# Kernel optimization log

Measured on AMD Instinct MI355X. Metric: run time of the kernel, lower is better.

## Reference

```python
import jax, jax.numpy as jnp
import numpy as np

N = 100000
E = 1600000
IN_CH = 128
HEADS = 4
OUT_CH = 32
NEG_SLOPE = 0.2


def setup_inputs() -> dict:
    key = jax.random.key(0)
    k1, k2, k3, k4 = jax.random.split(key, 4)
    x = jax.random.normal(k1, (N, IN_CH), dtype=jnp.float32)
    edge_index = jax.random.randint(k2, (2, E), 0, N, dtype=jnp.int64)
    # xavier-uniform-like init scales
    w_lim = float(np.sqrt(6.0 / (IN_CH + HEADS * OUT_CH)))
    a_lim = float(np.sqrt(6.0 / (HEADS + 2 * OUT_CH)))
    weight = jax.random.uniform(k3, (IN_CH, HEADS * OUT_CH), dtype=jnp.float32, minval=-w_lim, maxval=w_lim)
    att = jax.random.uniform(k4, (1, HEADS, 2 * OUT_CH), dtype=jnp.float32, minval=-a_lim, maxval=a_lim)
    bias = jnp.zeros((HEADS * OUT_CH,), dtype=jnp.float32)
    return {"x": x, "edge_index": edge_index, "weight": weight, "att": att, "bias": bias}


def reference(x, edge_index, weight, att, bias):
    n = x.shape[0]
    h = jnp.matmul(x, weight).reshape(n, HEADS, OUT_CH)  # [N, H, C]
    src, dst = edge_index[0], edge_index[1]
    x_src = h[src]  # [E, H, C]
    x_dst = h[dst]  # [E, H, C]
    # att is [1, H, 2C]; split so we never materialize the concat tensor
    att_src = att[:, :, :OUT_CH]  # [1, H, C]
    att_dst = att[:, :, OUT_CH:]  # [1, H, C]
    alpha = (x_src * att_src).sum(-1) + (x_dst * att_dst).sum(-1)  # [E, H]
    alpha = jnp.where(alpha >= 0, alpha, NEG_SLOPE * alpha)  # leaky_relu
    # segment softmax over edges grouped by dst
    seg_max = jax.ops.segment_max(alpha, dst, num_segments=n)  # [N, H]
    alpha = jnp.exp(alpha - seg_max[dst])
    seg_sum = jax.ops.segment_sum(alpha, dst, num_segments=n)  # [N, H]
    alpha = alpha / (seg_sum[dst] + 1e-16)
    # scatter-add weighted messages
    out = jax.ops.segment_sum(alpha[:, :, None] * x_src, dst, num_segments=n)  # [N, H, C]
    out = out.reshape(n, HEADS * OUT_CH)  # concat=True
    return out + bias
```

## Files before the change

kernel.cpp:

```cpp
#include <hip/hip_runtime.h>

#define N_NODES 100000
#define N_EDGES 1600000
#define IN_CH   128
#define HEADS   4
#define OUT_CH  32
#define HID     128
#define NEG_SLOPE 0.2f

#define BNODES  1024
#define NBUCK   ((N_NODES + BNODES - 1) / BNODES)
#define NBLK    256
#define EPB     (N_EDGES / NBLK)
#define BSLOT   18432

typedef unsigned int  uint;
typedef unsigned short ushort;

__device__ __forceinline__ ushort f2bf(float f) {
    uint u = __float_as_uint(f);
    return (ushort)((u + 0x7FFFu + ((u >> 16) & 1u)) >> 16);
}

#define BM 64
#define BK 32
__global__ __launch_bounds__(256) void k_gemm(const float* __restrict__ x,
                                              const float* __restrict__ w,
                                              const float* __restrict__ att,
                                              ushort* __restrict__ h,
                                              float* __restrict__ s_src,
                                              float* __restrict__ s_dst,
                                              int* __restrict__ bucket_cnt) {
    __shared__ float xs[BK][BM + 4];
    __shared__ float wsld[BK][HID + 4];

    const int tid  = threadIdx.x;
    const int nodeBase = blockIdx.x * BM;
    const int c0 = (tid & 15) * 8;
    const int n0 = (tid >> 4) * 4;

    if (blockIdx.x == 0 && tid < NBUCK) bucket_cnt[tid] = 0;

    float acc[4][8];
#pragma unroll
    for (int i = 0; i < 4; i++)
#pragma unroll
        for (int j = 0; j < 8; j++) acc[i][j] = 0.0f;

    for (int k0 = 0; k0 < IN_CH; k0 += BK) {
#pragma unroll
        for (int l = 0; l < 2; l++) {
            int idx  = tid + l * 256;
            int row  = idx >> 3;
            int col4 = (idx & 7) * 4;
            int n = nodeBase + row;
            float4 v = make_float4(0.f, 0.f, 0.f, 0.f);
            if (n < N_NODES) v = *reinterpret_cast<const float4*>(x + (size_t)n * IN_CH + k0 + col4);
            xs[col4 + 0][row] = v.x;
            xs[col4 + 1][row] = v.y;
            xs[col4 + 2][row] = v.z;
            xs[col4 + 3][row] = v.w;
        }
#pragma unroll
        for (int l = 0; l < 4; l++) {
            int idx  = tid + l * 256;
            int row  = idx >> 5;
            int col4 = (idx & 31) * 4;
            float4 v = *reinterpret_cast<const float4*>(w + (size_t)(k0 + row) * HID + col4);
            *reinterpret_cast<float4*>(&wsld[row][col4]) = v;
        }
        __syncthreads();

#pragma unroll
        for (int kk = 0; kk < BK; kk++) {
            float4 xv = *reinterpret_cast<const float4*>(&xs[kk][n0]);
            float4 wa = *reinterpret_cast<const float4*>(&wsld[kk][c0]);
            float4 wb = *reinterpret_cast<const float4*>(&wsld[kk][c0 + 4]);
            float xr[4] = {xv.x, xv.y, xv.z, xv.w};
            float wr[8] = {wa.x, wa.y, wa.z, wa.w, wb.x, wb.y, wb.z, wb.w};
#pragma unroll
            for (int i = 0; i < 4; i++)
#pragma unroll
                for (int j = 0; j < 8; j++)
                    acc[i][j] = fmaf(xr[i], wr[j], acc[i][j]);
        }
        __syncthreads();
    }

#pragma unroll
    for (int i = 0; i < 4; i++) {
        int n = nodeBase + n0 + i;
        if (n < N_NODES) {
            uint4 pk;
            pk.x = (uint)f2bf(acc[i][0]) | ((uint)f2bf(acc[i][1]) << 16);
            pk.y = (uint)f2bf(acc[i][2]) | ((uint)f2bf(acc[i][3]) << 16);
            pk.z = (uint)f2bf(acc[i][4]) | ((uint)f2bf(acc[i][5]) << 16);
            pk.w = (uint)f2bf(acc[i][6]) | ((uint)f2bf(acc[i][7]) << 16);
            *reinterpret_cast<uint4*>(h + (size_t)n * HID + c0) = pk;
        }
    }

    {
        const int head = c0 >> 5;
        const int cb   = c0 & 31;
        const float* as = att + head * (2 * OUT_CH) + cb;
        const float* ad = as + OUT_CH;
        float av[8], dv[8];
#pragma unroll
        for (int j = 0; j < 8; j++) { av[j] = as[j]; dv[j] = ad[j]; }
#pragma unroll
        for (int i = 0; i < 4; i++) {
            float ps = 0.f, pd = 0.f;
#pragma unroll
            for (int j = 0; j < 8; j++) {
                ps = fmaf(acc[i][j], av[j], ps);
                pd = fmaf(acc[i][j], dv[j], pd);
            }
            ps += __shfl_xor(ps, 1);  ps += __shfl_xor(ps, 2);
            pd += __shfl_xor(pd, 1);  pd += __shfl_xor(pd, 2);
            int n = nodeBase + n0 + i;
            if ((tid & 3) == 0 && n < N_NODES) {
                s_src[n * HEADS + head] = ps;
                s_dst[n * HEADS + head] = pd;
            }
        }
    }
}

__global__ __launch_bounds__(256) void k_scatter(const int* __restrict__ ei,
                                                 int* __restrict__ bucket_cnt,
                                                 int* __restrict__ packed) {
    __shared__ int cnt[NBUCK];
    __shared__ int cur[NBUCK];
    int t = threadIdx.x;
    if (t < NBUCK) cnt[t] = 0;
    __syncthreads();
    int base = blockIdx.x * EPB;
    for (int e = base + t; e < base + EPB; e += 256)
        atomicAdd(&cnt[ei[N_EDGES + e] >> 10], 1);
    __syncthreads();
    if (t < NBUCK) {
        int myBase = atomicAdd(&bucket_cnt[t], cnt[t]);
        cur[t] = t * BSLOT + myBase;
    }
    __syncthreads();
    for (int e = base + t; e < base + EPB; e += 256) {
        int src = ei[e], dst = ei[N_EDGES + e];
        int pos = atomicAdd(&cur[dst >> 10], 1);
        packed[pos] = (src << 10) | (dst & (BNODES - 1));
    }
}

__global__ __launch_bounds__(256) void k_b2(const int* __restrict__ packed,
                                            const int* __restrict__ bucket_cnt,
                                            int* __restrict__ csr_src,
                                            int* __restrict__ row_start) {
    __shared__ int cnt[BNODES];
    __shared__ int cur[BNODES];
    __shared__ int sm[256];
    int b = blockIdx.x, t = threadIdx.x;

    sm[t] = (t < NBUCK) ? bucket_cnt[t] : 0;
    __syncthreads();
    for (int off = 1; off < 256; off <<= 1) {
        int v = (t >= off) ? sm[t - off] : 0;
        __syncthreads();
        sm[t] += v;
        __syncthreads();
    }
    int myCnt     = bucket_cnt[b];
    int tight_beg = sm[b] - myCnt;
    int beg_pad   = b * BSLOT;
    int end_pad   = beg_pad + myCnt;
    __syncthreads();

#pragma unroll
    for (int j = 0; j < 4; j++) cnt[t * 4 + j] = 0;
    __syncthreads();
    for (int e = beg_pad + t; e < end_pad; e += 256)
        atomicAdd(&cnt[packed[e] & (BNODES - 1)], 1);
    __syncthreads();
    int c0 = cnt[t * 4], c1 = cnt[t * 4 + 1], c2 = cnt[t * 4 + 2], c3 = cnt[t * 4 + 3];
    int tot = c0 + c1 + c2 + c3;
    sm[t] = tot;
    __syncthreads();
    for (int off = 1; off < 256; off <<= 1) {
        int v = (t >= off) ? sm[t - off] : 0;
        __syncthreads();
        sm[t] += v;
        __syncthreads();
    }
    int p0 = tight_beg + sm[t] - tot;
    int p1 = p0 + c0, p2 = p1 + c1, p3 = p2 + c2;
    cur[t * 4] = p0; cur[t * 4 + 1] = p1; cur[t * 4 + 2] = p2; cur[t * 4 + 3] = p3;
    int nodeb = b * BNODES + t * 4;
    int pv[4] = {p0, p1, p2, p3};
#pragma unroll
    for (int j = 0; j < 4; j++)
        if (nodeb + j <= N_NODES) row_start[nodeb + j] = pv[j];
    __syncthreads();
    for (int e = beg_pad + t; e < end_pad; e += 256) {
        int pk = packed[e];
        int pos = atomicAdd(&cur[pk & (BNODES - 1)], 1);
        csr_src[pos] = pk >> 10;
    }
}

__global__ __launch_bounds__(256) void k_agg(const int* __restrict__ row_start,
                                             const int* __restrict__ csr_src,
                                             const float* __restrict__ s_src,
                                             const float* __restrict__ s_dst,
                                             const ushort* __restrict__ h,
                                             const float* __restrict__ bias,
                                             float* __restrict__ out) {
    const int n    = blockIdx.x * 4 + (threadIdx.x >> 6);
    const int lane = threadIdx.x & 63;
    const int g    = lane >> 4;
    const int q    = lane & 15;
    const int head = q >> 2;

    const float sdh = s_dst[n * HEADS + head];
    const int beg = row_start[n], end = row_start[n + 1];
    const uint4* __restrict__ hrow = reinterpret_cast<const uint4*>(h);

    float acc[8];
#pragma unroll
    for (int k = 0; k < 8; k++) acc[k] = 0.f;
    float sum_w = 0.f;

#pragma unroll 2
    for (int j = beg; j < end; j += 4) {
        int e = j + g;
        bool valid = e < end;
        int src = csr_src[valid ? e : end - 1];
        float ss = s_src[src * HEADS + head];
        uint4 u = hrow[(size_t)src * (HID / 8) + q];
        float a = ss + sdh;
        a = fmaxf(a, NEG_SLOPE * a);
        float wgt = valid ? __expf(a) : 0.f;
        sum_w += wgt;
        uint uv[4] = {u.x, u.y, u.z, u.w};
#pragma unroll
        for (int t = 0; t < 4; t++) {
            acc[2 * t]     = fmaf(wgt, __uint_as_float(uv[t] << 16),        acc[2 * t]);
            acc[2 * t + 1] = fmaf(wgt, __uint_as_float(uv[t] & 0xFFFF0000u), acc[2 * t + 1]);
        }
    }

#pragma unroll
    for (int k = 0; k < 8; k++) {
        acc[k] += __shfl_xor(acc[k], 16);
        acc[k] += __shfl_xor(acc[k], 32);
    }
    sum_w += __shfl_xor(sum_w, 16);
    sum_w += __shfl_xor(sum_w, 32);

    if (g == 0) {
        float inv = 1.0f / (sum_w + 1e-16f);
        int ch = q * 8;
        float4 b0 = *reinterpret_cast<const float4*>(bias + ch);
        float4 b1 = *reinterpret_cast<const float4*>(bias + ch + 4);
        float4 o0, o1;
        o0.x = acc[0] * inv + b0.x; o0.y = acc[1] * inv + b0.y;
        o0.z = acc[2] * inv + b0.z; o0.w = acc[3] * inv + b0.w;
        o1.x = acc[4] * inv + b1.x; o1.y = acc[5] * inv + b1.y;
        o1.z = acc[6] * inv + b1.z; o1.w = acc[7] * inv + b1.w;
        *reinterpret_cast<float4*>(out + (size_t)n * HID + ch)     = o0;
        *reinterpret_cast<float4*>(out + (size_t)n * HID + ch + 4) = o1;
    }
}

extern "C" void kernel_launch(void* const* d_in, const int* in_sizes, int n_in,
                              void* d_out, int out_size, void* d_ws, size_t ws_size,
                              hipStream_t stream) {
    const float* x    = (const float*)d_in[0];
    const int*   ei   = (const int*)  d_in[1];
    const float* w    = (const float*)d_in[2];
    const float* att  = (const float*)d_in[3];
    const float* bias = (const float*)d_in[4];
    float* out = (float*)d_out;

    char* p = (char*)d_ws;
    float* s_src    = (float*)p;  p += (size_t)N_NODES * HEADS * 4;
    float* s_dst    = (float*)p;  p += (size_t)N_NODES * HEADS * 4;
    ushort* h       = (ushort*)p; p += (size_t)N_NODES * HID * 2;
    int* csr_src    = (int*)p;    p += (size_t)N_EDGES * 4;
    int* packed     = (int*)p;    p += (size_t)NBUCK * BSLOT * 4;
    int* row_start  = (int*)p;    p += (size_t)(N_NODES + 1) * 4;
    int* bucket_cnt = (int*)p;    p += (size_t)NBUCK * 4;

    k_gemm<<<(N_NODES + BM - 1) / BM, 256, 0, stream>>>(x, w, att, h, s_src, s_dst, bucket_cnt);
    k_scatter<<<NBLK, 256, 0, stream>>>(ei, bucket_cnt, packed);
    k_b2<<<NBUCK, 256, 0, stream>>>(packed, bucket_cnt, csr_src, row_start);
    k_agg<<<N_NODES / 4, 256, 0, stream>>>(row_start, csr_src, s_src, s_dst, h, bias, out);
}
```

Measured before the change: 301.8 us.

## Enlarge GEMM tile with register prefetch, halve bucket size, cache dst in registers

The projection GEMM moves to 128-node tiles with an 8x8 register block per thread. It prefetches the next K-slice into registers while computing the current one and stores x in a XOR-swizzled shared-memory layout to avoid bank conflicts. The attention-score reduction is rewritten to match the new thread mapping. Buckets for the CSR build shrink from 1024 to 512 nodes, and the scatter kernel keeps each edge's dst in registers so it is not reloaded on the second pass. Costs are higher register pressure in the GEMM and more, smaller buckets in the two-level sort.

```diff
diff --git a/kernel.cpp b/kernel.cpp
--- a/kernel.cpp
+++ b/kernel.cpp
@@ -8,11 +8,11 @@
 #define HID     128
 #define NEG_SLOPE 0.2f
 
-#define BNODES  1024
+#define BNODES  512
 #define NBUCK   ((N_NODES + BNODES - 1) / BNODES)
 #define NBLK    256
 #define EPB     (N_EDGES / NBLK)
-#define BSLOT   18432
+#define BSLOT   9216
 
 typedef unsigned int  uint;
 typedef unsigned short ushort;
@@ -22,7 +22,7 @@
     return (ushort)((u + 0x7FFFu + ((u >> 16) & 1u)) >> 16);
 }
 
-#define BM 64
+#define BM 128
 #define BK 32
 __global__ __launch_bounds__(256) void k_gemm(const float* __restrict__ x,
                                               const float* __restrict__ w,
@@ -31,98 +31,119 @@
                                               float* __restrict__ s_src,
                                               float* __restrict__ s_dst,
                                               int* __restrict__ bucket_cnt) {
-    __shared__ float xs[BK][BM + 4];
+    __shared__ float xsw[BK * BM];
     __shared__ float wsld[BK][HID + 4];
 
-    const int tid  = threadIdx.x;
+    const int tid = threadIdx.x;
     const int nodeBase = blockIdx.x * BM;
-    const int c0 = (tid & 15) * 8;
-    const int n0 = (tid >> 4) * 4;
+    const int q   = tid & 15;
+    const int v8  = (tid >> 4) * 8;
+    const int cLo = q * 4;
+    const int cHi = 64 + q * 4;
 
     if (blockIdx.x == 0 && tid < NBUCK) bucket_cnt[tid] = 0;
 
-    float acc[4][8];
-#pragma unroll
-    for (int i = 0; i < 4; i++)
+    float acc[8][8];
+#pragma unroll
+    for (int i = 0; i < 8; i++)
 #pragma unroll
         for (int j = 0; j < 8; j++) acc[i][j] = 0.0f;
 
-    for (int k0 = 0; k0 < IN_CH; k0 += BK) {
-#pragma unroll
-        for (int l = 0; l < 2; l++) {
-            int idx  = tid + l * 256;
-            int row  = idx >> 3;
-            int col4 = (idx & 7) * 4;
-            int n = nodeBase + row;
-            float4 v = make_float4(0.f, 0.f, 0.f, 0.f);
-            if (n < N_NODES) v = *reinterpret_cast<const float4*>(x + (size_t)n * IN_CH + k0 + col4);
-            xs[col4 + 0][row] = v.x;
-            xs[col4 + 1][row] = v.y;
-            xs[col4 + 2][row] = v.z;
-            xs[col4 + 3][row] = v.w;
-        }
+    const int s_nl  = tid >> 3;
+    const int s_c4  = (tid & 7) * 4;
+    const int s_row = tid >> 5;
+    const int s_co  = (tid & 31) * 4;
+
+    float4 xp[4], wp[4];
+#pragma unroll
+    for (int l = 0; l < 4; l++) {
+        int nl = s_nl + 32 * l;
+        int n  = nodeBase + nl;
+        xp[l] = (n < N_NODES) ? *reinterpret_cast<const float4*>(x + (size_t)n * IN_CH + s_c4)
+                              : make_float4(0.f, 0.f, 0.f, 0.f);
+        wp[l] = *reinterpret_cast<const float4*>(w + (size_t)(s_row + 8 * l) * HID + s_co);
+    }
+
+    for (int t = 0; t < 4; t++) {
+        if (t) __syncthreads();
 #pragma unroll
         for (int l = 0; l < 4; l++) {
-            int idx  = tid + l * 256;
-            int row  = idx >> 5;
-            int col4 = (idx & 31) * 4;
-            float4 v = *reinterpret_cast<const float4*>(w + (size_t)(k0 + row) * HID + col4);
-            *reinterpret_cast<float4*>(&wsld[row][col4]) = v;
-        }
-        __syncthreads();
+            int nl = s_nl + 32 * l;
+            int flip = (((tid & 7) ^ ((nl >> 5) & 3)) << 2);
+            float vv[4] = {xp[l].x, xp[l].y, xp[l].z, xp[l].w};
+#pragma unroll
+            for (int j = 0; j < 4; j++)
+                xsw[(((s_c4 + j) << 7) + nl) ^ flip] = vv[j];
+            *reinterpret_cast<float4*>(&wsld[s_row + 8 * l][s_co]) = wp[l];
+        }
+        __syncthreads();
+
+        if (t < 3) {
+            int k0n = (t + 1) * BK;
+#pragma unroll
+            for (int l = 0; l < 4; l++) {
+                int nl = s_nl + 32 * l;
+                int n  = nodeBase + nl;
+                xp[l] = (n < N_NODES) ? *reinterpret_cast<const float4*>(x + (size_t)n * IN_CH + k0n + s_c4)
+                                      : make_float4(0.f, 0.f, 0.f, 0.f);
+                wp[l] = *reinterpret_cast<const float4*>(w + (size_t)(k0n + s_row + 8 * l) * HID + s_co);
+            }
+        }
 
 #pragma unroll
         for (int kk = 0; kk < BK; kk++) {
-            float4 xv = *reinterpret_cast<const float4*>(&xs[kk][n0]);
-            float4 wa = *reinterpret_cast<const float4*>(&wsld[kk][c0]);
-            float4 wb = *reinterpret_cast<const float4*>(&wsld[kk][c0 + 4]);
-            float xr[4] = {xv.x, xv.y, xv.z, xv.w};
-            float wr[8] = {wa.x, wa.y, wa.z, wa.w, wb.x, wb.y, wb.z, wb.w};
-#pragma unroll
-            for (int i = 0; i < 4; i++)
+            int fl = ((((kk >> 2) & 7) ^ ((v8 >> 5) & 3)) << 2);
+            float4 xlo = *reinterpret_cast<const float4*>(&xsw[((kk << 7) + v8) ^ fl]);
+            float4 xhi = *reinterpret_cast<const float4*>(&xsw[((kk << 7) + v8 + 4) ^ fl]);
+            float4 wlo = *reinterpret_cast<const float4*>(&wsld[kk][cLo]);
+            float4 whi = *reinterpret_cast<const float4*>(&wsld[kk][cHi]);
+            float xr[8] = {xlo.x, xlo.y, xlo.z, xlo.w, xhi.x, xhi.y, xhi.z, xhi.w};
+            float wr[8] = {wlo.x, wlo.y, wlo.z, wlo.w, whi.x, whi.y, whi.z, whi.w};
+#pragma unroll
+            for (int i = 0; i < 8; i++)
 #pragma unroll
                 for (int j = 0; j < 8; j++)
                     acc[i][j] = fmaf(xr[i], wr[j], acc[i][j]);
         }
-        __syncthreads();
-    }
-
-#pragma unroll
-    for (int i = 0; i < 4; i++) {
-        int n = nodeBase + n0 + i;
-        if (n < N_NODES) {
-            uint4 pk;
-            pk.x = (uint)f2bf(acc[i][0]) | ((uint)f2bf(acc[i][1]) << 16);
-            pk.y = (uint)f2bf(acc[i][2]) | ((uint)f2bf(acc[i][3]) << 16);
-            pk.z = (uint)f2bf(acc[i][4]) | ((uint)f2bf(acc[i][5]) << 16);
-            pk.w = (uint)f2bf(acc[i][6]) | ((uint)f2bf(acc[i][7]) << 16);
-            *reinterpret_cast<uint4*>(h + (size_t)n * HID + c0) = pk;
-        }
-    }
-
-    {
-        const int head = c0 >> 5;
-        const int cb   = c0 & 31;
-        const float* as = att + head * (2 * OUT_CH) + cb;
-        const float* ad = as + OUT_CH;
-        float av[8], dv[8];
-#pragma unroll
-        for (int j = 0; j < 8; j++) { av[j] = as[j]; dv[j] = ad[j]; }
-#pragma unroll
-        for (int i = 0; i < 4; i++) {
-            float ps = 0.f, pd = 0.f;
-#pragma unroll
-            for (int j = 0; j < 8; j++) {
-                ps = fmaf(acc[i][j], av[j], ps);
-                pd = fmaf(acc[i][j], dv[j], pd);
-            }
-            ps += __shfl_xor(ps, 1);  ps += __shfl_xor(ps, 2);
-            pd += __shfl_xor(pd, 1);  pd += __shfl_xor(pd, 2);
-            int n = nodeBase + n0 + i;
-            if ((tid & 3) == 0 && n < N_NODES) {
-                s_src[n * HEADS + head] = ps;
-                s_dst[n * HEADS + head] = pd;
-            }
+    }
+
+    const int head_lo = (tid >> 3) & 1;
+    const int head_hi = head_lo + 2;
+    const int cbase   = 4 * (tid & 7);
+    float4 aslo = *reinterpret_cast<const float4*>(att + head_lo * 64 + cbase);
+    float4 adlo = *reinterpret_cast<const float4*>(att + head_lo * 64 + 32 + cbase);
+    float4 ashi = *reinterpret_cast<const float4*>(att + head_hi * 64 + cbase);
+    float4 adhi = *reinterpret_cast<const float4*>(att + head_hi * 64 + 32 + cbase);
+
+#pragma unroll
+    for (int i = 0; i < 8; i++) {
+        int n = nodeBase + v8 + i;
+        bool ok = (n < N_NODES);
+        if (ok) {
+            uint2 plo, phi;
+            plo.x = (uint)f2bf(acc[i][0]) | ((uint)f2bf(acc[i][1]) << 16);
+            plo.y = (uint)f2bf(acc[i][2]) | ((uint)f2bf(acc[i][3]) << 16);
+            phi.x = (uint)f2bf(acc[i][4]) | ((uint)f2bf(acc[i][5]) << 16);
+            phi.y = (uint)f2bf(acc[i][6]) | ((uint)f2bf(acc[i][7]) << 16);
+            *reinterpret_cast<uint2*>(h + (size_t)n * HID + cLo) = plo;
+            *reinterpret_cast<uint2*>(h + (size_t)n * HID + cHi) = phi;
+        }
+        float sl_s = acc[i][0]*aslo.x + acc[i][1]*aslo.y + acc[i][2]*aslo.z + acc[i][3]*aslo.w;
+        float sl_d = acc[i][0]*adlo.x + acc[i][1]*adlo.y + acc[i][2]*adlo.z + acc[i][3]*adlo.w;
+        float sh_s = acc[i][4]*ashi.x + acc[i][5]*ashi.y + acc[i][6]*ashi.z + acc[i][7]*ashi.w;
+        float sh_d = acc[i][4]*adhi.x + acc[i][5]*adhi.y + acc[i][6]*adhi.z + acc[i][7]*adhi.w;
+#pragma unroll
+        for (int off = 1; off < 8; off <<= 1) {
+            sl_s += __shfl_xor(sl_s, off);
+            sl_d += __shfl_xor(sl_d, off);
+            sh_s += __shfl_xor(sh_s, off);
+            sh_d += __shfl_xor(sh_d, off);
+        }
+        if ((tid & 7) == 0 && ok) {
+            s_src[n * HEADS + head_lo] = sl_s;
+            s_dst[n * HEADS + head_lo] = sl_d;
+            s_src[n * HEADS + head_hi] = sh_s;
+            s_dst[n * HEADS + head_hi] = sh_d;
         }
     }
 }
@@ -136,18 +157,30 @@
     if (t < NBUCK) cnt[t] = 0;
     __syncthreads();
     int base = blockIdx.x * EPB;
-    for (int e = base + t; e < base + EPB; e += 256)
-        atomicAdd(&cnt[ei[N_EDGES + e] >> 10], 1);
+    int dreg[25];
+#pragma unroll
+    for (int j = 0; j < 25; j++) {
+        bool ok = (j < 24) || (t < EPB - 24 * 256);
+        int e = base + t + j * 256;
+        dreg[j] = ok ? ei[N_EDGES + e] : -1;
+        if (ok) atomicAdd(&cnt[dreg[j] >> 9], 1);
+    }
     __syncthreads();
     if (t < NBUCK) {
         int myBase = atomicAdd(&bucket_cnt[t], cnt[t]);
         cur[t] = t * BSLOT + myBase;
     }
     __syncthreads();
-    for (int e = base + t; e < base + EPB; e += 256) {
-        int src = ei[e], dst = ei[N_EDGES + e];
-        int pos = atomicAdd(&cur[dst >> 10], 1);
-        packed[pos] = (src << 10) | (dst & (BNODES - 1));
+#pragma unroll
+    for (int j = 0; j < 25; j++) {
+        bool ok = (j < 24) || (t < EPB - 24 * 256);
+        if (ok) {
+            int e = base + t + j * 256;
+            int src = ei[e];
+            int d   = dreg[j];
+            int pos = atomicAdd(&cur[d >> 9], 1);
+            packed[pos] = (src << 9) | (d & (BNODES - 1));
+        }
     }
 }
 
@@ -175,13 +208,13 @@
     __syncthreads();
 
 #pragma unroll
-    for (int j = 0; j < 4; j++) cnt[t * 4 + j] = 0;
+    for (int j = 0; j < 2; j++) cnt[t * 2 + j] = 0;
     __syncthreads();
     for (int e = beg_pad + t; e < end_pad; e += 256)
         atomicAdd(&cnt[packed[e] & (BNODES - 1)], 1);
     __syncthreads();
-    int c0 = cnt[t * 4], c1 = cnt[t * 4 + 1], c2 = cnt[t * 4 + 2], c3 = cnt[t * 4 + 3];
-    int tot = c0 + c1 + c2 + c3;
+    int c0 = cnt[t * 2], c1 = cnt[t * 2 + 1];
+    int tot = c0 + c1;
     sm[t] = tot;
     __syncthreads();
     for (int off = 1; off < 256; off <<= 1) {
@@ -191,18 +224,16 @@
         __syncthreads();
     }
     int p0 = tight_beg + sm[t] - tot;
-    int p1 = p0 + c0, p2 = p1 + c1, p3 = p2 + c2;
-    cur[t * 4] = p0; cur[t * 4 + 1] = p1; cur[t * 4 + 2] = p2; cur[t * 4 + 3] = p3;
-    int nodeb = b * BNODES + t * 4;
-    int pv[4] = {p0, p1, p2, p3};
-#pragma unroll
-    for (int j = 0; j < 4; j++)
-        if (nodeb + j <= N_NODES) row_start[nodeb + j] = pv[j];
+    int p1 = p0 + c0;
+    cur[t * 2] = p0; cur[t * 2 + 1] = p1;
+    int nodeb = b * BNODES + t * 2;
+    if (nodeb     <= N_NODES) row_start[nodeb]     = p0;
+    if (nodeb + 1 <= N_NODES) row_start[nodeb + 1] = p1;
     __syncthreads();
     for (int e = beg_pad + t; e < end_pad; e += 256) {
         int pk = packed[e];
         int pos = atomicAdd(&cur[pk & (BNODES - 1)], 1);
-        csr_src[pos] = pk >> 10;
+        csr_src[pos] = pk >> 9;
     }
 }
 
```

Measured after the change: 327.2 us. +8.4%, slower.
